# Kernel optimization log

Measured on AMD Instinct MI355X. Metric: run time of the kernel, lower is better.

The kernel has to match this reference:

```python
import jax, jax.numpy as jnp
import numpy as np

EPS = 1e-6  # EPSILON in the original (undefined there; small stabilizer)
MS = 1      # max_shift_size
FEAT = 128  # memory_feature_size


def setup_inputs() -> dict:
    key = jax.random.key(0)
    ks = jax.random.split(key, 17)
    B, V, E, H, N, F = 64, 10000, 256, 512, 8192, FEAT
    G = 4 * H
    s = 0.02  # param init scale
    return {
        'x': jax.random.randint(ks[0], (B,), 0, V),
        'h': jax.random.normal(ks[1], (B, H)) * 0.1,
        'c': jax.random.normal(ks[2], (B, H)) * 0.1,
        'w_read': jax.random.uniform(ks[3], (B, N)),
        'w_write': jax.random.uniform(ks[4], (B, N)),
        'bank': jax.random.normal(ks[5], (B, N, F)),
        'emb': jax.random.normal(ks[6], (V, E)) * s,
        'W_ih': jax.random.normal(ks[7], (G, E)) * s,
        'b_ih': jnp.zeros((G,)),
        'W_hh': jax.random.normal(ks[8], (G, H)) * s,
        'b_hh': jnp.zeros((G,)),
        'W_read': jax.random.normal(ks[9], (134, H)) * s,
        'b_read': jnp.zeros((134,)),
        'W_write': jax.random.normal(ks[10], (390, H)) * s,
        'b_write': jnp.zeros((390,)),
        'W_out': jax.random.normal(ks[11], (V, F)) * s,
        'b_out': jnp.zeros((V,)),
    }


def _lstm_cell(xe, h, c, W_ih, b_ih, W_hh, b_hh):
    g = xe @ W_ih.T + b_ih + h @ W_hh.T + b_hh  # [B, 4H]
    i, f, gg, o = jnp.split(g, 4, axis=1)
    c2 = jax.nn.sigmoid(f) * c + jax.nn.sigmoid(i) * jnp.tanh(gg)
    h2 = jax.nn.sigmoid(o) * jnp.tanh(c2)
    return h2, c2


def _head_move(bank, w_prev, k, b, g, s, r):
    # content addressing: cosine similarity of key vs each memory row
    mE = bank + EPS                       # [B, N, F]
    kE = k[:, None, :] + EPS              # [B, 1, F]
    num = jnp.sum(mE * kE, axis=-1)       # [B, N]
    den = jnp.linalg.norm(mE, axis=-1) * jnp.linalg.norm(kE, axis=-1)
    sim = num / jnp.maximum(den, 1e-8)
    w = jax.nn.softmax(b * sim, axis=1)
    # interpolation (as written in the source: w + (1-g)*w_prev)
    w = w + (1.0 - g) * w_prev
    # circular shift by location addressing (vectorized conv over modulo pad)
    N = w.shape[1]
    idx = (jnp.arange(N)[:, None] + jnp.arange(-MS, MS + 1)[None, :]) % N  # [N, K]
    w = jnp.einsum('bnk,bk->bn', w[:, idx], s)
    # sharpen
    wr = w ** r
    return wr / (jnp.sum(wr, axis=1, keepdims=True) + EPS)


def _interpret_read(h, W, b):
    o = h @ W.T + b
    F = FEAT
    k = o[:, :F]
    beta = jax.nn.softplus(o[:, F:F + 1])
    g = jax.nn.sigmoid(o[:, F + 1:F + 2])
    s = jax.nn.softmax(o[:, F + 2:F + 2 + (2 * MS + 1)], axis=1)
    r = 1.0 + jax.nn.softplus(o[:, F + 2 + (2 * MS + 1):F + 3 + (2 * MS + 1)])
    return k, beta, g, s, r


def _interpret_write(h, W, b):
    o = h @ W.T + b
    F = FEAT
    k, beta, g, s, r = _interpret_read(h, W[:F + 3 + (2 * MS + 1)], b[:F + 3 + (2 * MS + 1)])
    base = F + 3 + (2 * MS + 1)
    e = jax.nn.sigmoid(o[:, base:base + F])
    a = o[:, base + F:base + 2 * F]
    return k, beta, g, s, r, e, a


def reference(x, h, c, w_read, w_write, bank, emb, W_ih, b_ih, W_hh, b_hh,
              W_read, b_read, W_write, b_write, W_out, b_out):
    # controller
    xe = emb[x]                                  # [B, E]
    h2, c2 = _lstm_cell(xe, h, c, W_ih, b_ih, W_hh, b_hh)
    # write head + memory write
    k, beta, g, s, r, e, a = _interpret_write(h2, W_write, b_write)
    ww = _head_move(bank, w_write, k, beta, g, s, r)   # [B, N]
    bank2 = bank * (1.0 - ww[:, :, None] * e[:, None, :]) + ww[:, :, None] * a[:, None, :]
    # read head + memory read (uses updated bank)
    k, beta, g, s, r = _interpret_read(h2, W_read, b_read)
    wr = _head_move(bank2, w_read, k, beta, g, s, r)
    rvec = jnp.sum(wr[:, :, None] * bank2, axis=1)     # [B, F]
    return rvec @ W_out.T + b_out                      # [B, V]
```

## Files before the change

kernel.cpp:

```cpp
#include <hip/hip_runtime.h>
#include <math.h>

#define BB   64
#define NN   8192
#define FF   128
#define HH   512
#define GG   2048
#define EE   256
#define VV   10000
#define EPSF 1e-6f

static constexpr size_t OFF_XT    = 0;
static constexpr size_t OFF_GPART = 49152;
static constexpr size_t OFF_H2T   = 311296;
static constexpr size_t OFF_HPART = 344064;
static constexpr size_t OFF_PAR   = 411136;
static constexpr size_t OFF_ZW    = 445952;
static constexpr size_t OFF_Q4    = 970240;
static constexpr size_t OFF_Q1    = 3067392;
static constexpr size_t OFF_WR    = 3591680;
static constexpr size_t OFF_WRWW  = 4115968;
static constexpr size_t OFF_PT    = 4640256;
static constexpr size_t OFF_T3    = 5164544;
static constexpr size_t OFF_RVEC  = 5164608;

__device__ __forceinline__ float sigmoidf_(float x){ return 1.f/(1.f + __expf(-x)); }
__device__ __forceinline__ float softplusf_(float x){ return (x > 20.f) ? x : log1pf(__expf(x)); }

__global__ __launch_bounds__(256) void gather_xt_kernel(
    const int* __restrict__ x, const float* __restrict__ h,
    const float* __restrict__ emb, float* __restrict__ Xt)
{
  const int idx = blockIdx.x*256 + threadIdx.x;
  const int k = idx >> 6, b = idx & 63;
  float v = (k < EE) ? emb[(size_t)x[b]*EE + k] : h[(size_t)b*HH + (k - EE)];
  Xt[(size_t)k*64 + b] = v;
}

__global__ __launch_bounds__(256) void lstm_gates_kernel(
    const float* __restrict__ Xt, const float* __restrict__ Wih,
    const float* __restrict__ Whh, float* __restrict__ gpart)
{
  const int tid = threadIdx.x;
  const int lane = tid & 63;
  const int gw = __builtin_amdgcn_readfirstlane(blockIdx.x*4 + (tid >> 6));
  const int jg = gw >> 1, kc = gw & 1;
  const int j0 = jg << 2;
  float a0=0.f, a1=0.f, a2=0.f, a3=0.f;
  if (kc == 0){
    const float* w0 = Wih + (size_t)(j0+0)*EE;
    const float* w1 = Wih + (size_t)(j0+1)*EE;
    const float* w2 = Wih + (size_t)(j0+2)*EE;
    const float* w3 = Wih + (size_t)(j0+3)*EE;
    #pragma unroll 4
    for (int k = 0; k < EE; ++k){
      const float xv = Xt[(size_t)k*64 + lane];
      a0 = fmaf(w0[k],xv,a0); a1 = fmaf(w1[k],xv,a1);
      a2 = fmaf(w2[k],xv,a2); a3 = fmaf(w3[k],xv,a3);
    }
    const float* v0 = Whh + (size_t)(j0+0)*HH;
    const float* v1 = Whh + (size_t)(j0+1)*HH;
    const float* v2 = Whh + (size_t)(j0+2)*HH;
    const float* v3 = Whh + (size_t)(j0+3)*HH;
    #pragma unroll 4
    for (int k = 0; k < 128; ++k){
      const float xv = Xt[(size_t)(EE+k)*64 + lane];
      a0 = fmaf(v0[k],xv,a0); a1 = fmaf(v1[k],xv,a1);
      a2 = fmaf(v2[k],xv,a2); a3 = fmaf(v3[k],xv,a3);
    }
  } else {
    const float* v0 = Whh + (size_t)(j0+0)*HH;
    const float* v1 = Whh + (size_t)(j0+1)*HH;
    const float* v2 = Whh + (size_t)(j0+2)*HH;
    const float* v3 = Whh + (size_t)(j0+3)*HH;
    #pragma unroll 4
    for (int k = 128; k < 512; ++k){
      const float xv = Xt[(size_t)(EE+k)*64 + lane];
      a0 = fmaf(v0[k],xv,a0); a1 = fmaf(v1[k],xv,a1);
      a2 = fmaf(v2[k],xv,a2); a3 = fmaf(v3[k],xv,a3);
    }
  }
  float* gp = gpart + (size_t)kc*131072 + (size_t)j0*64 + lane;
  gp[0] = a0; gp[64] = a1; gp[128] = a2; gp[192] = a3;
}

__global__ __launch_bounds__(256) void lstm_act_kernel(
    const float* __restrict__ gpart, const float* __restrict__ bih,
    const float* __restrict__ bhh, const float* __restrict__ c,
    float* __restrict__ h2t)
{
  const int idx = blockIdx.x*256 + threadIdx.x;
  const int bb = idx & 63, hh = idx >> 6;
  #define GSUM(j) (gpart[(size_t)(j)*64+bb] + gpart[(size_t)131072+(size_t)(j)*64+bb] + bih[j] + bhh[j])
  const float gi = GSUM(hh);
  const float gf = GSUM(512+hh);
  const float gg = GSUM(1024+hh);
  const float go = GSUM(1536+hh);
  #undef GSUM
  const float c0 = c[(size_t)bb*HH + hh];
  const float c2 = sigmoidf_(gf)*c0 + sigmoidf_(gi)*tanhf(gg);
  h2t[(size_t)hh*64 + bb] = sigmoidf_(go)*tanhf(c2);
}

__global__ __launch_bounds__(256) void head_gemm_kernel(
    const float* __restrict__ h2t, const float* __restrict__ Ww,
    const float* __restrict__ Wr, float* __restrict__ hpart)
{
  const int tid = threadIdx.x;
  const int lane = tid & 63;
  const int gw = __builtin_amdgcn_readfirstlane(blockIdx.x*4 + (tid >> 6));
  const int jg = gw >> 1, kc = gw & 1;
  if (jg >= 131) return;
  const int j0 = jg << 2;
  const float* w0 = (j0+0 < 390) ? (Ww + (size_t)(j0+0)*HH) : (Wr + (size_t)(j0+0-390)*HH);
  const float* w1 = (j0+1 < 390) ? (Ww + (size_t)(j0+1)*HH) : (Wr + (size_t)(j0+1-390)*HH);
  const float* w2 = (j0+2 < 390) ? (Ww + (size_t)(j0+2)*HH) : (Wr + (size_t)(j0+2-390)*HH);
  const float* w3 = (j0+3 < 390) ? (Ww + (size_t)(j0+3)*HH) : (Wr + (size_t)(j0+3-390)*HH);
  const int k0 = kc << 8;
  float a0=0.f, a1=0.f, a2=0.f, a3=0.f;
  #pragma unroll 4
  for (int k = k0; k < k0+256; ++k){
    const float xv = h2t[(size_t)k*64 + lane];
    a0 = fmaf(w0[k],xv,a0); a1 = fmaf(w1[k],xv,a1);
    a2 = fmaf(w2[k],xv,a2); a3 = fmaf(w3[k],xv,a3);
  }
  float* hp = hpart + (size_t)kc*33536 + (size_t)j0*64 + lane;
  hp[0] = a0; hp[64] = a1; hp[128] = a2; hp[192] = a3;
}

__global__ void interpret_kernel(const float* __restrict__ hp,
                                 const float* __restrict__ bw,
                                 const float* __restrict__ br,
                                 float* __restrict__ params)
{
  const int b = blockIdx.x, l = threadIdx.x;
  float* P = params + (size_t)b*544;
  #define OC(j) (hp[(size_t)(j)*64+b] + hp[(size_t)33536+(size_t)(j)*64+b])
  float skw = 0.f, skr = 0.f, sakr = 0.f, sa2 = 0.f;
  #pragma unroll
  for (int f = l; f < 128; f += 64){
    float kwE = OC(f) + bw[f] + EPSF;
    float ee  = sigmoidf_(OC(134+f) + bw[134+f]);
    float aa  = OC(262+f) + bw[262+f];
    float krE = OC(390+f) + br[f] + EPSF;
    P[f] = kwE; P[128+f] = krE; P[256+f] = aa; P[384+f] = ee;
    skw = fmaf(kwE,kwE,skw); skr = fmaf(krE,krE,skr);
    sakr = fmaf(aa,krE,sakr); sa2 = fmaf(aa,aa,sa2);
  }
  #pragma unroll
  for (int m = 32; m >= 1; m >>= 1){
    skw += __shfl_xor(skw,m); skr += __shfl_xor(skr,m);
    sakr += __shfl_xor(sakr,m); sa2 += __shfl_xor(sa2,m);
  }
  if (l == 0){
    P[512+0] = softplusf_(OC(128) + bw[128]);
    P[512+1] = sigmoidf_(OC(129) + bw[129]);
    {
      float x0 = OC(130)+bw[130], x1 = OC(131)+bw[131], x2 = OC(132)+bw[132];
      float mm = fmaxf(x0, fmaxf(x1, x2));
      float e0 = __expf(x0-mm), e1 = __expf(x1-mm), e2 = __expf(x2-mm);
      float s = e0+e1+e2;
      P[512+2] = e0/s; P[512+3] = e1/s; P[512+4] = e2/s;
    }
    P[512+5] = 1.f + softplusf_(OC(133) + bw[133]);
    P[512+6] = softplusf_(OC(518) + br[128]);
    P[512+7] = sigmoidf_(OC(519) + br[129]);
    {
      float x0 = OC(520)+br[130], x1 = OC(521)+br[131], x2 = OC(522)+br[132];
      float mm = fmaxf(x0, fmaxf(x1, x2));
      float e0 = __expf(x0-mm), e1 = __expf(x1-mm), e2 = __expf(x2-mm);
      float s = e0+e1+e2;
      P[512+8] = e0/s; P[512+9] = e1/s; P[512+10] = e2/s;
    }
    P[512+11] = 1.f + softplusf_(OC(523) + br[133]);
    P[512+12] = sqrtf(skw); P[512+13] = sqrtf(skr);
    P[512+14] = sakr;       P[512+15] = sa2;
  }
  #undef OC
}

__global__ __launch_bounds__(256) void pass_a_kernel(
    const float* __restrict__ bank, const float* __restrict__ params,
    float* __restrict__ zw, float4* __restrict__ q4, float* __restrict__ q1)
{
  const int blk = blockIdx.x;
  const int b = blk >> 5, chunk = blk & 31;
  const int tid = threadIdx.x;
  const int wv = tid >> 6, lane = tid & 63;
  const int fslot = lane & 7, rsub = lane >> 3;
  const float* P = params + (size_t)b*544;
  float kw[16], kr[16], av[16], ev[16];
  #pragma unroll
  for (int i = 0; i < 4; ++i){
    #pragma unroll
    for (int j = 0; j < 4; ++j){
      const int idx = 32*i + 4*fslot + j;
      kw[4*i+j] = P[idx];     kr[4*i+j] = P[128+idx];
      av[4*i+j] = P[256+idx]; ev[4*i+j] = P[384+idx];
    }
  }
  const float beta_w = P[512+0], nkw = P[512+12];
  const float C_akr = P[512+14], Ca2 = P[512+15];
  const int eoff = 4*fslot;

  for (int it = 0; it < 8; it += 2){
    const int n0 = (chunk << 8) + (it << 5) + (wv << 3) + rsub;
    const size_t rowA = (size_t)b*NN + n0;
    const size_t rowB = rowA + 32;
    const float* pA = bank + rowA*FF + eoff;
    const float* pB = bank + rowB*FF + eoff;
    float va[16], vb[16];
    #pragma unroll
    for (int i = 0; i < 4; ++i)
      *reinterpret_cast<float4*>(&va[4*i]) = *reinterpret_cast<const float4*>(pA + 32*i);
    #pragma unroll
    for (int i = 0; i < 4; ++i)
      *reinterpret_cast<float4*>(&vb[4*i]) = *reinterpret_cast<const float4*>(pB + 32*i);

    #pragma unroll
    for (int half = 0; half < 2; ++half){
      const float* mv = (half == 0) ? va : vb;
      const size_t row = (half == 0) ? rowA : rowB;
      float s1=0.f,s2=0.f,s3=0.f,s4=0.f,s5=0.f,s6=0.f,s7=0.f,s8=0.f;
      #pragma unroll
      for (int i = 0; i < 16; ++i){
        const float m = mv[i], u = m + EPSF, em = ev[i]*m;
        s1 = fmaf(u,kw[i],s1);  s2 = fmaf(u,u,s2);
        s3 = fmaf(u,kr[i],s3);  s4 = fmaf(em,kr[i],s4);
        s5 = fmaf(u,av[i],s5);  s6 = fmaf(u,em,s6);
        s7 = fmaf(av[i],em,s7); s8 = fmaf(em,em,s8);
      }
      #pragma unroll
      for (int mm = 1; mm < 8; mm <<= 1){
        s1 += __shfl_xor(s1,mm); s2 += __shfl_xor(s2,mm);
        s3 += __shfl_xor(s3,mm); s4 += __shfl_xor(s4,mm);
        s5 += __shfl_xor(s5,mm); s6 += __shfl_xor(s6,mm);
        s7 += __shfl_xor(s7,mm); s8 += __shfl_xor(s8,mm);
      }
      if (fslot == 0){
        const float sim = s1 / fmaxf(sqrtf(s2)*nkw, 1e-8f);
        zw[row] = beta_w * sim;
        q4[row] = make_float4(s2, s3, C_akr - s4, s5 - s6);
        q1[row] = Ca2 - 2.f*s7 + s8;
      }
    }
  }
}

__device__ __forceinline__ float blockMaxF(float v, float* red, int tid){
  #pragma unroll
  for (int m = 32; m >= 1; m >>= 1) v = fmaxf(v, __shfl_xor(v,m));
  if ((tid & 63) == 0) red[tid >> 6] = v;
  __syncthreads();
  if (tid < 64){
    float x = (tid < 16) ? red[tid] : -1e30f;
    #pragma unroll
    for (int m = 8; m >= 1; m >>= 1) x = fmaxf(x, __shfl_xor(x,m));
    if (tid == 0) red[16] = x;
  }
  __syncthreads();
  return red[16];
}
__device__ __forceinline__ float blockSumF(float v, float* red, int tid){
  #pragma unroll
  for (int m = 32; m >= 1; m >>= 1) v += __shfl_xor(v,m);
  if ((tid & 63) == 0) red[tid >> 6] = v;
  __syncthreads();
  if (tid < 64){
    float x = (tid < 16) ? red[tid] : 0.f;
    #pragma unroll
    for (int m = 8; m >= 1; m >>= 1) x += __shfl_xor(x,m);
    if (tid == 0) red[16] = x;
  }
  __syncthreads();
  return red[16];
}

__global__ __launch_bounds__(1024) void head_pipeline_kernel(
    const float* __restrict__ zw, const float4* __restrict__ q4,
    const float* __restrict__ q1,
    const float* __restrict__ w_write, const float* __restrict__ w_read,
    const float* __restrict__ params,
    float* __restrict__ wrg, float* __restrict__ wrwwg, float* __restrict__ T3g)
{
  __shared__ float wa[NN];
  __shared__ float red[20];
  const int b = blockIdx.x;
  const int tid = threadIdx.x;
  const float* P = params + (size_t)b*544 + 512;
  const float g_w = P[1], sw0 = P[2], sw1 = P[3], sw2 = P[4], r_w = P[5];
  const float beta_r = P[6], g_r = P[7], sr0 = P[8], sr1 = P[9], sr2 = P[10], r_r = P[11];
  const float nkr = P[13];
  const size_t base = (size_t)b*NN;

  float  zv[8], q1v[8], wwr[8], wrd[8];
  float4 qv[8];
  #pragma unroll
  for (int i = 0; i < 8; ++i){ int n = tid + (i<<10); zv[i]  = zw[base+n]; }
  #pragma unroll
  for (int i = 0; i < 8; ++i){ int n = tid + (i<<10); qv[i]  = q4[base+n]; }
  #pragma unroll
  for (int i = 0; i < 8; ++i){ int n = tid + (i<<10); q1v[i] = q1[base+n]; }
  #pragma unroll
  for (int i = 0; i < 8; ++i){ int n = tid + (i<<10); wwr[i] = w_write[base+n]; }
  #pragma unroll
  for (int i = 0; i < 8; ++i){ int n = tid + (i<<10); wrd[i] = w_read[base+n]; }

  float cv[8], wwv[8];

  float lm = -1e30f;
  #pragma unroll
  for (int i = 0; i < 8; ++i) lm = fmaxf(lm, zv[i]);
  float M = blockMaxF(lm, red, tid);
  float ls = 0.f;
  #pragma unroll
  for (int i = 0; i < 8; ++i){ zv[i] = __expf(zv[i]-M); ls += zv[i]; }
  float S = blockSumF(ls, red, tid);
  const float invS = 1.f/S;
  #pragma unroll
  for (int i = 0; i < 8; ++i){ int n = tid + (i<<10); wa[n] = zv[i]*invS + (1.f-g_w)*wwr[i]; }
  __syncthreads();
  #pragma unroll
  for (int i = 0; i < 8; ++i){ int n = tid + (i<<10);
    cv[i] = sw0*wa[(n+NN-1)&(NN-1)] + sw1*wa[n] + sw2*wa[(n+1)&(NN-1)]; }
  __syncthreads();
  float lp = 0.f;
  #pragma unroll
  for (int i = 0; i < 8; ++i){ cv[i] = __expf(r_w*__logf(cv[i])); lp += cv[i]; }
  float Sp = blockSumF(lp, red, tid);
  float inv = 1.f/(Sp + EPSF);
  #pragma unroll
  for (int i = 0; i < 8; ++i) wwv[i] = cv[i]*inv;

  lm = -1e30f;
  #pragma unroll
  for (int i = 0; i < 8; ++i){
    const float ww = wwv[i];
    const float num = qv[i].y + ww*qv[i].z;
    const float d2  = qv[i].x + 2.f*ww*qv[i].w + ww*ww*q1v[i];
    const float den = sqrtf(d2)*nkr;
    zv[i] = beta_r * (num / fmaxf(den, 1e-8f));
    lm = fmaxf(lm, zv[i]);
  }
  M = blockMaxF(lm, red, tid);
  ls = 0.f;
  #pragma unroll
  for (int i = 0; i < 8; ++i){ zv[i] = __expf(zv[i]-M); ls += zv[i]; }
  S = blockSumF(ls, red, tid);
  const float invS2 = 1.f/S;
  #pragma unroll
  for (int i = 0; i < 8; ++i){ int n = tid + (i<<10); wa[n] = zv[i]*invS2 + (1.f-g_r)*wrd[i]; }
  __syncthreads();
  #pragma unroll
  for (int i = 0; i < 8; ++i){ int n = tid + (i<<10);
    cv[i] = sr0*wa[(n+NN-1)&(NN-1)] + sr1*wa[n] + sr2*wa[(n+1)&(NN-1)]; }
  __syncthreads();
  float lp2 = 0.f;
  #pragma unroll
  for (int i = 0; i < 8; ++i){ cv[i] = __expf(r_r*__logf(cv[i])); lp2 += cv[i]; }
  float Sp2 = blockSumF(lp2, red, tid);
  inv = 1.f/(Sp2 + EPSF);
  float t3 = 0.f;
  #pragma unroll
  for (int i = 0; i < 8; ++i){
    int n = tid + (i<<10);
    const float wr_ = cv[i]*inv;
    wrg[base+n] = wr_;
    const float xx = wr_*wwv[i];
    wrwwg[base+n] = xx;
    t3 += xx;
  }
  float T3 = blockSumF(t3, red, tid);
  if (tid == 0) T3g[b] = T3;
}

__global__ __launch_bounds__(256) void pass_d_kernel(
    const float* __restrict__ bank, const float* __restrict__ wrg,
    const float* __restrict__ wrwwg, float* __restrict__ pT)
{
  const int blk = 2047 - blockIdx.x;
  const int b = blk >> 5, chunk = blk & 31;
  const int tid = threadIdx.x;
  const int st = tid >> 5, li = tid & 31;
  float4 a1 = make_float4(0.f,0.f,0.f,0.f);
  float4 a2 = make_float4(0.f,0.f,0.f,0.f);
  for (int it = 28; it >= 0; it -= 4){
    float w1v[4], w2v[4];
    float4 mv[4];
    #pragma unroll
    for (int u = 0; u < 4; ++u){
      const int n = (chunk << 8) + ((it+u) << 3) + st;
      const size_t row = (size_t)b*NN + n;
      w1v[u] = wrg[row];
      w2v[u] = wrwwg[row];
      mv[u] = reinterpret_cast<const float4*>(bank + row*FF)[li];
    }
    #pragma unroll
    for (int u = 0; u < 4; ++u){
      a1.x = fmaf(w1v[u],mv[u].x,a1.x); a1.y = fmaf(w1v[u],mv[u].y,a1.y);
      a1.z = fmaf(w1v[u],mv[u].z,a1.z); a1.w = fmaf(w1v[u],mv[u].w,a1.w);
      a2.x = fmaf(w2v[u],mv[u].x,a2.x); a2.y = fmaf(w2v[u],mv[u].y,a2.y);
      a2.z = fmaf(w2v[u],mv[u].z,a2.z); a2.w = fmaf(w2v[u],mv[u].w,a2.w);
    }
  }
  __shared__ float lds[8*256];
  *reinterpret_cast<float4*>(&lds[st*256 + li*4]) = a1;
  *reinterpret_cast<float4*>(&lds[st*256 + 128 + li*4]) = a2;
  __syncthreads();
  float s = 0.f;
  #pragma unroll
  for (int k = 0; k < 8; ++k) s += lds[k*256 + tid];
  pT[(size_t)blk*256 + tid] = s;
}

__global__ __launch_bounds__(256) void rvec_kernel(
    const float* __restrict__ pT, const float* __restrict__ params,
    const float* __restrict__ T3g, float* __restrict__ rvec)
{
  const int gid = blockIdx.x*256 + threadIdx.x;
  const int b = gid >> 7, f = gid & 127;
  float t1 = 0.f, t2 = 0.f;
  for (int cc = 0; cc < 32; ++cc){
    const float* p = pT + (size_t)((b<<5) + cc)*256;
    t1 += p[f]; t2 += p[128+f];
  }
  const float* P = params + (size_t)b*544;
  rvec[gid] = t1 - P[384+f]*t2 + P[256+f]*T3g[b];
}

__global__ __launch_bounds__(256) void out_gemm_kernel(
    const float* __restrict__ rvec, const float* __restrict__ Wout,
    const float* __restrict__ bout, float* __restrict__ out)
{
  const int tid = threadIdx.x;
  const int wv = __builtin_amdgcn_readfirstlane(tid >> 6);
  const int lane = tid & 63;
  const int j0 = blockIdx.x*32 + wv*8;
  float acc[8];
  #pragma unroll
  for (int jj = 0; jj < 8; ++jj){ int j = j0 + jj; acc[jj] = (j < VV) ? bout[j] : 0.f; }
  for (int fc = 0; fc < 128; fc += 32){
    float rv[32];
    #pragma unroll
    for (int i = 0; i < 32; ++i) rv[i] = rvec[lane*128 + fc + i];
    #pragma unroll
    for (int jj = 0; jj < 8; ++jj){
      const int j = j0 + jj;
      if (j < VV){
        const float* w = Wout + (size_t)j*128 + fc;
        #pragma unroll
        for (int i = 0; i < 32; ++i) acc[jj] = fmaf(w[i], rv[i], acc[jj]);
      }
    }
  }
  #pragma unroll
  for (int jj = 0; jj < 8; ++jj){
    int j = j0 + jj;
    if (j < VV) out[(size_t)lane*VV + j] = acc[jj];
  }
}

extern "C" void kernel_launch(void* const* d_in, const int* in_sizes, int n_in,
                              void* d_out, int out_size, void* d_ws, size_t ws_size,
                              hipStream_t stream)
{
  const int*   x       = (const int*)  d_in[0];
  const float* h       = (const float*)d_in[1];
  const float* c       = (const float*)d_in[2];
  const float* w_read  = (const float*)d_in[3];
  const float* w_write = (const float*)d_in[4];
  const float* bank    = (const float*)d_in[5];
  const float* emb     = (const float*)d_in[6];
  const float* Wih     = (const float*)d_in[7];
  const float* bih     = (const float*)d_in[8];
  const float* Whh     = (const float*)d_in[9];
  const float* bhh     = (const float*)d_in[10];
  const float* Wr      = (const float*)d_in[11];
  const float* br      = (const float*)d_in[12];
  const float* Ww      = (const float*)d_in[13];
  const float* bw      = (const float*)d_in[14];
  const float* Wout    = (const float*)d_in[15];
  const float* bout    = (const float*)d_in[16];
  float* out = (float*)d_out;
  float* ws  = (float*)d_ws;

  float* Xt    = ws + OFF_XT;
  float* gpart = ws + OFF_GPART;
  float* h2t   = ws + OFF_H2T;
  float* hpart = ws + OFF_HPART;
  float* par   = ws + OFF_PAR;
  float* zwp   = ws + OFF_ZW;
  float4* q4p  = reinterpret_cast<float4*>(ws + OFF_Q4);
  float* q1p   = ws + OFF_Q1;
  float* wrp   = ws + OFF_WR;
  float* wrwwp = ws + OFF_WRWW;
  float* pTp   = ws + OFF_PT;
  float* T3p   = ws + OFF_T3;
  float* rvp   = ws + OFF_RVEC;

  hipLaunchKernelGGL(gather_xt_kernel,     dim3(192),  dim3(256), 0, stream, x, h, emb, Xt);
  hipLaunchKernelGGL(lstm_gates_kernel,    dim3(256),  dim3(256), 0, stream, Xt, Wih, Whh, gpart);
  hipLaunchKernelGGL(lstm_act_kernel,      dim3(128),  dim3(256), 0, stream, gpart, bih, bhh, c, h2t);
  hipLaunchKernelGGL(head_gemm_kernel,     dim3(66),   dim3(256), 0, stream, h2t, Ww, Wr, hpart);
  hipLaunchKernelGGL(interpret_kernel,     dim3(64),   dim3(64),  0, stream, hpart, bw, br, par);
  hipLaunchKernelGGL(pass_a_kernel,        dim3(2048), dim3(256), 0, stream, bank, par, zwp, q4p, q1p);
  hipLaunchKernelGGL(head_pipeline_kernel, dim3(64),   dim3(1024),0, stream, zwp, q4p, q1p, w_write, w_read, par, wrp, wrwwp, T3p);
  hipLaunchKernelGGL(pass_d_kernel,        dim3(2048), dim3(256), 0, stream, bank, wrp, wrwwp, pTp);
  hipLaunchKernelGGL(rvec_kernel,          dim3(32),   dim3(256), 0, stream, pTp, par, T3p, rvp);
  hipLaunchKernelGGL(out_gemm_kernel,      dim3(313),  dim3(256), 0, stream, rvp, Wout, bout, out);
}
```

Baseline: 196.5 us.

## Fuse controller and head-parameter kernels into one cooperative kernel with grid syncs

Merges the five small pre-processing kernels (embedding gather, LSTM gates, LSTM activation, head GEMM, interpret) into a single cooperative launch of 256 blocks, using grid-wide syncs between the stages. The aim is to remove four kernel launch boundaries and their gaps on these tiny latency-bound stages. In exchange it adds grid.sync barriers, which carry their own cost, and it depends on all 256 blocks being co-resident for the cooperative launch.

```diff
diff --git a/kernel.cpp b/kernel.cpp
--- a/kernel.cpp
+++ b/kernel.cpp
@@ -1,5 +1,8 @@
 #include <hip/hip_runtime.h>
+#include <hip/hip_cooperative_groups.h>
 #include <math.h>
+
+namespace cg = cooperative_groups;
 
 #define BB   64
 #define NN   8192
@@ -27,156 +30,157 @@
 __device__ __forceinline__ float sigmoidf_(float x){ return 1.f/(1.f + __expf(-x)); }
 __device__ __forceinline__ float softplusf_(float x){ return (x > 20.f) ? x : log1pf(__expf(x)); }
 
-__global__ __launch_bounds__(256) void gather_xt_kernel(
+__global__ __launch_bounds__(256) void fused_pre_kernel(
     const int* __restrict__ x, const float* __restrict__ h,
-    const float* __restrict__ emb, float* __restrict__ Xt)
-{
-  const int idx = blockIdx.x*256 + threadIdx.x;
-  const int k = idx >> 6, b = idx & 63;
-  float v = (k < EE) ? emb[(size_t)x[b]*EE + k] : h[(size_t)b*HH + (k - EE)];
-  Xt[(size_t)k*64 + b] = v;
-}
-
-__global__ __launch_bounds__(256) void lstm_gates_kernel(
-    const float* __restrict__ Xt, const float* __restrict__ Wih,
-    const float* __restrict__ Whh, float* __restrict__ gpart)
-{
-  const int tid = threadIdx.x;
+    const float* __restrict__ emb,
+    const float* __restrict__ Wih, const float* __restrict__ bih,
+    const float* __restrict__ Whh, const float* __restrict__ bhh,
+    const float* __restrict__ c,
+    const float* __restrict__ Ww, const float* __restrict__ bw,
+    const float* __restrict__ Wr, const float* __restrict__ br,
+    float* __restrict__ Xt, float* __restrict__ gpart,
+    float* __restrict__ h2t, float* __restrict__ hpart,
+    float* __restrict__ params)
+{
+  cg::grid_group grid = cg::this_grid();
+  const int tid  = threadIdx.x;
+  const int gtid = blockIdx.x*256 + tid;
   const int lane = tid & 63;
-  const int gw = __builtin_amdgcn_readfirstlane(blockIdx.x*4 + (tid >> 6));
-  const int jg = gw >> 1, kc = gw & 1;
-  const int j0 = jg << 2;
-  float a0=0.f, a1=0.f, a2=0.f, a3=0.f;
-  if (kc == 0){
-    const float* w0 = Wih + (size_t)(j0+0)*EE;
-    const float* w1 = Wih + (size_t)(j0+1)*EE;
-    const float* w2 = Wih + (size_t)(j0+2)*EE;
-    const float* w3 = Wih + (size_t)(j0+3)*EE;
-    #pragma unroll 4
-    for (int k = 0; k < EE; ++k){
-      const float xv = Xt[(size_t)k*64 + lane];
-      a0 = fmaf(w0[k],xv,a0); a1 = fmaf(w1[k],xv,a1);
-      a2 = fmaf(w2[k],xv,a2); a3 = fmaf(w3[k],xv,a3);
-    }
-    const float* v0 = Whh + (size_t)(j0+0)*HH;
-    const float* v1 = Whh + (size_t)(j0+1)*HH;
-    const float* v2 = Whh + (size_t)(j0+2)*HH;
-    const float* v3 = Whh + (size_t)(j0+3)*HH;
-    #pragma unroll 4
-    for (int k = 0; k < 128; ++k){
-      const float xv = Xt[(size_t)(EE+k)*64 + lane];
-      a0 = fmaf(v0[k],xv,a0); a1 = fmaf(v1[k],xv,a1);
-      a2 = fmaf(v2[k],xv,a2); a3 = fmaf(v3[k],xv,a3);
-    }
-  } else {
-    const float* v0 = Whh + (size_t)(j0+0)*HH;
-    const float* v1 = Whh + (size_t)(j0+1)*HH;
-    const float* v2 = Whh + (size_t)(j0+2)*HH;
-    const float* v3 = Whh + (size_t)(j0+3)*HH;
-    #pragma unroll 4
-    for (int k = 128; k < 512; ++k){
-      const float xv = Xt[(size_t)(EE+k)*64 + lane];
-      a0 = fmaf(v0[k],xv,a0); a1 = fmaf(v1[k],xv,a1);
-      a2 = fmaf(v2[k],xv,a2); a3 = fmaf(v3[k],xv,a3);
-    }
-  }
-  float* gp = gpart + (size_t)kc*131072 + (size_t)j0*64 + lane;
-  gp[0] = a0; gp[64] = a1; gp[128] = a2; gp[192] = a3;
-}
-
-__global__ __launch_bounds__(256) void lstm_act_kernel(
-    const float* __restrict__ gpart, const float* __restrict__ bih,
-    const float* __restrict__ bhh, const float* __restrict__ c,
-    float* __restrict__ h2t)
-{
-  const int idx = blockIdx.x*256 + threadIdx.x;
-  const int bb = idx & 63, hh = idx >> 6;
-  #define GSUM(j) (gpart[(size_t)(j)*64+bb] + gpart[(size_t)131072+(size_t)(j)*64+bb] + bih[j] + bhh[j])
-  const float gi = GSUM(hh);
-  const float gf = GSUM(512+hh);
-  const float gg = GSUM(1024+hh);
-  const float go = GSUM(1536+hh);
-  #undef GSUM
-  const float c0 = c[(size_t)bb*HH + hh];
-  const float c2 = sigmoidf_(gf)*c0 + sigmoidf_(gi)*tanhf(gg);
-  h2t[(size_t)hh*64 + bb] = sigmoidf_(go)*tanhf(c2);
-}
-
-__global__ __launch_bounds__(256) void head_gemm_kernel(
-    const float* __restrict__ h2t, const float* __restrict__ Ww,
-    const float* __restrict__ Wr, float* __restrict__ hpart)
-{
-  const int tid = threadIdx.x;
-  const int lane = tid & 63;
-  const int gw = __builtin_amdgcn_readfirstlane(blockIdx.x*4 + (tid >> 6));
-  const int jg = gw >> 1, kc = gw & 1;
-  if (jg >= 131) return;
-  const int j0 = jg << 2;
-  const float* w0 = (j0+0 < 390) ? (Ww + (size_t)(j0+0)*HH) : (Wr + (size_t)(j0+0-390)*HH);
-  const float* w1 = (j0+1 < 390) ? (Ww + (size_t)(j0+1)*HH) : (Wr + (size_t)(j0+1-390)*HH);
-  const float* w2 = (j0+2 < 390) ? (Ww + (size_t)(j0+2)*HH) : (Wr + (size_t)(j0+2-390)*HH);
-  const float* w3 = (j0+3 < 390) ? (Ww + (size_t)(j0+3)*HH) : (Wr + (size_t)(j0+3-390)*HH);
-  const int k0 = kc << 8;
-  float a0=0.f, a1=0.f, a2=0.f, a3=0.f;
-  #pragma unroll 4
-  for (int k = k0; k < k0+256; ++k){
-    const float xv = h2t[(size_t)k*64 + lane];
-    a0 = fmaf(w0[k],xv,a0); a1 = fmaf(w1[k],xv,a1);
-    a2 = fmaf(w2[k],xv,a2); a3 = fmaf(w3[k],xv,a3);
-  }
-  float* hp = hpart + (size_t)kc*33536 + (size_t)j0*64 + lane;
-  hp[0] = a0; hp[64] = a1; hp[128] = a2; hp[192] = a3;
-}
-
-__global__ void interpret_kernel(const float* __restrict__ hp,
-                                 const float* __restrict__ bw,
-                                 const float* __restrict__ br,
-                                 float* __restrict__ params)
-{
-  const int b = blockIdx.x, l = threadIdx.x;
-  float* P = params + (size_t)b*544;
-  #define OC(j) (hp[(size_t)(j)*64+b] + hp[(size_t)33536+(size_t)(j)*64+b])
-  float skw = 0.f, skr = 0.f, sakr = 0.f, sa2 = 0.f;
-  #pragma unroll
-  for (int f = l; f < 128; f += 64){
-    float kwE = OC(f) + bw[f] + EPSF;
-    float ee  = sigmoidf_(OC(134+f) + bw[134+f]);
-    float aa  = OC(262+f) + bw[262+f];
-    float krE = OC(390+f) + br[f] + EPSF;
-    P[f] = kwE; P[128+f] = krE; P[256+f] = aa; P[384+f] = ee;
-    skw = fmaf(kwE,kwE,skw); skr = fmaf(krE,krE,skr);
-    sakr = fmaf(aa,krE,sakr); sa2 = fmaf(aa,aa,sa2);
-  }
-  #pragma unroll
-  for (int m = 32; m >= 1; m >>= 1){
-    skw += __shfl_xor(skw,m); skr += __shfl_xor(skr,m);
-    sakr += __shfl_xor(sakr,m); sa2 += __shfl_xor(sa2,m);
-  }
-  if (l == 0){
-    P[512+0] = softplusf_(OC(128) + bw[128]);
-    P[512+1] = sigmoidf_(OC(129) + bw[129]);
-    {
-      float x0 = OC(130)+bw[130], x1 = OC(131)+bw[131], x2 = OC(132)+bw[132];
-      float mm = fmaxf(x0, fmaxf(x1, x2));
-      float e0 = __expf(x0-mm), e1 = __expf(x1-mm), e2 = __expf(x2-mm);
-      float s = e0+e1+e2;
-      P[512+2] = e0/s; P[512+3] = e1/s; P[512+4] = e2/s;
-    }
-    P[512+5] = 1.f + softplusf_(OC(133) + bw[133]);
-    P[512+6] = softplusf_(OC(518) + br[128]);
-    P[512+7] = sigmoidf_(OC(519) + br[129]);
-    {
-      float x0 = OC(520)+br[130], x1 = OC(521)+br[131], x2 = OC(522)+br[132];
-      float mm = fmaxf(x0, fmaxf(x1, x2));
-      float e0 = __expf(x0-mm), e1 = __expf(x1-mm), e2 = __expf(x2-mm);
-      float s = e0+e1+e2;
-      P[512+8] = e0/s; P[512+9] = e1/s; P[512+10] = e2/s;
-    }
-    P[512+11] = 1.f + softplusf_(OC(523) + br[133]);
-    P[512+12] = sqrtf(skw); P[512+13] = sqrtf(skr);
-    P[512+14] = sakr;       P[512+15] = sa2;
-  }
-  #undef OC
+
+  if (gtid < 49152){
+    const int k = gtid >> 6, b = gtid & 63;
+    float v = (k < EE) ? emb[(size_t)x[b]*EE + k] : h[(size_t)b*HH + (k - EE)];
+    Xt[(size_t)k*64 + b] = v;
+  }
+  grid.sync();
+
+  {
+    const int gw = __builtin_amdgcn_readfirstlane(blockIdx.x*4 + (tid >> 6));
+    const int jg = gw >> 1, kc = gw & 1;
+    const int j0 = jg << 2;
+    float a0=0.f, a1=0.f, a2=0.f, a3=0.f;
+    if (kc == 0){
+      const float* w0 = Wih + (size_t)(j0+0)*EE;
+      const float* w1 = Wih + (size_t)(j0+1)*EE;
+      const float* w2 = Wih + (size_t)(j0+2)*EE;
+      const float* w3 = Wih + (size_t)(j0+3)*EE;
+      #pragma unroll 4
+      for (int k = 0; k < EE; ++k){
+        const float xv = Xt[(size_t)k*64 + lane];
+        a0 = fmaf(w0[k],xv,a0); a1 = fmaf(w1[k],xv,a1);
+        a2 = fmaf(w2[k],xv,a2); a3 = fmaf(w3[k],xv,a3);
+      }
+      const float* v0 = Whh + (size_t)(j0+0)*HH;
+      const float* v1 = Whh + (size_t)(j0+1)*HH;
+      const float* v2 = Whh + (size_t)(j0+2)*HH;
+      const float* v3 = Whh + (size_t)(j0+3)*HH;
+      #pragma unroll 4
+      for (int k = 0; k < 128; ++k){
+        const float xv = Xt[(size_t)(EE+k)*64 + lane];
+        a0 = fmaf(v0[k],xv,a0); a1 = fmaf(v1[k],xv,a1);
+        a2 = fmaf(v2[k],xv,a2); a3 = fmaf(v3[k],xv,a3);
+      }
+    } else {
+      const float* v0 = Whh + (size_t)(j0+0)*HH;
+      const float* v1 = Whh + (size_t)(j0+1)*HH;
+      const float* v2 = Whh + (size_t)(j0+2)*HH;
+      const float* v3 = Whh + (size_t)(j0+3)*HH;
+      #pragma unroll 4
+      for (int k = 128; k < 512; ++k){
+        const float xv = Xt[(size_t)(EE+k)*64 + lane];
+        a0 = fmaf(v0[k],xv,a0); a1 = fmaf(v1[k],xv,a1);
+        a2 = fmaf(v2[k],xv,a2); a3 = fmaf(v3[k],xv,a3);
+      }
+    }
+    float* gp = gpart + (size_t)kc*131072 + (size_t)j0*64 + lane;
+    gp[0] = a0; gp[64] = a1; gp[128] = a2; gp[192] = a3;
+  }
+  grid.sync();
+
+  if (gtid < 32768){
+    const int bb = gtid & 63, hh = gtid >> 6;
+    #define GSUM(j) (gpart[(size_t)(j)*64+bb] + gpart[(size_t)131072+(size_t)(j)*64+bb] + bih[j] + bhh[j])
+    const float gi = GSUM(hh);
+    const float gf = GSUM(512+hh);
+    const float gg = GSUM(1024+hh);
+    const float go = GSUM(1536+hh);
+    #undef GSUM
+    const float c0 = c[(size_t)bb*HH + hh];
+    const float c2 = sigmoidf_(gf)*c0 + sigmoidf_(gi)*tanhf(gg);
+    h2t[(size_t)hh*64 + bb] = sigmoidf_(go)*tanhf(c2);
+  }
+  grid.sync();
+
+  {
+    const int gw = __builtin_amdgcn_readfirstlane(blockIdx.x*4 + (tid >> 6));
+    const int jg = gw >> 1, kc = gw & 1;
+    if (jg < 131){
+      const int j0 = jg << 2;
+      const float* w0 = (j0+0 < 390) ? (Ww + (size_t)(j0+0)*HH) : (Wr + (size_t)(j0+0-390)*HH);
+      const float* w1 = (j0+1 < 390) ? (Ww + (size_t)(j0+1)*HH) : (Wr + (size_t)(j0+1-390)*HH);
+      const float* w2 = (j0+2 < 390) ? (Ww + (size_t)(j0+2)*HH) : (Wr + (size_t)(j0+2-390)*HH);
+      const float* w3 = (j0+3 < 390) ? (Ww + (size_t)(j0+3)*HH) : (Wr + (size_t)(j0+3-390)*HH);
+      const int k0 = kc << 8;
+      float a0=0.f, a1=0.f, a2=0.f, a3=0.f;
+      #pragma unroll 4
+      for (int k = k0; k < k0+256; ++k){
+        const float xv = h2t[(size_t)k*64 + lane];
+        a0 = fmaf(w0[k],xv,a0); a1 = fmaf(w1[k],xv,a1);
+        a2 = fmaf(w2[k],xv,a2); a3 = fmaf(w3[k],xv,a3);
+      }
+      float* hp = hpart + (size_t)kc*33536 + (size_t)j0*64 + lane;
+      hp[0] = a0; hp[64] = a1; hp[128] = a2; hp[192] = a3;
+    }
+  }
+  grid.sync();
+
+  if (blockIdx.x < 64 && tid < 64){
+    const int b = blockIdx.x, l = tid;
+    const float* hp = hpart;
+    float* P = params + (size_t)b*544;
+    #define OC(j) (hp[(size_t)(j)*64+b] + hp[(size_t)33536+(size_t)(j)*64+b])
+    float skw = 0.f, skr = 0.f, sakr = 0.f, sa2 = 0.f;
+    #pragma unroll
+    for (int f = l; f < 128; f += 64){
+      float kwE = OC(f) + bw[f] + EPSF;
+      float ee  = sigmoidf_(OC(134+f) + bw[134+f]);
+      float aa  = OC(262+f) + bw[262+f];
+      float krE = OC(390+f) + br[f] + EPSF;
+      P[f] = kwE; P[128+f] = krE; P[256+f] = aa; P[384+f] = ee;
+      skw = fmaf(kwE,kwE,skw); skr = fmaf(krE,krE,skr);
+      sakr = fmaf(aa,krE,sakr); sa2 = fmaf(aa,aa,sa2);
+    }
+    #pragma unroll
+    for (int m = 32; m >= 1; m >>= 1){
+      skw += __shfl_xor(skw,m); skr += __shfl_xor(skr,m);
+      sakr += __shfl_xor(sakr,m); sa2 += __shfl_xor(sa2,m);
+    }
+    if (l == 0){
+      P[512+0] = softplusf_(OC(128) + bw[128]);
+      P[512+1] = sigmoidf_(OC(129) + bw[129]);
+      {
+        float x0 = OC(130)+bw[130], x1 = OC(131)+bw[131], x2 = OC(132)+bw[132];
+        float mm = fmaxf(x0, fmaxf(x1, x2));
+        float e0 = __expf(x0-mm), e1 = __expf(x1-mm), e2 = __expf(x2-mm);
+        float s = e0+e1+e2;
+        P[512+2] = e0/s; P[512+3] = e1/s; P[512+4] = e2/s;
+      }
+      P[512+5] = 1.f + softplusf_(OC(133) + bw[133]);
+      P[512+6] = softplusf_(OC(518) + br[128]);
+      P[512+7] = sigmoidf_(OC(519) + br[129]);
+      {
+        float x0 = OC(520)+br[130], x1 = OC(521)+br[131], x2 = OC(522)+br[132];
+        float mm = fmaxf(x0, fmaxf(x1, x2));
+        float e0 = __expf(x0-mm), e1 = __expf(x1-mm), e2 = __expf(x2-mm);
+        float s = e0+e1+e2;
+        P[512+8] = e0/s; P[512+9] = e1/s; P[512+10] = e2/s;
+      }
+      P[512+11] = 1.f + softplusf_(OC(523) + br[133]);
+      P[512+12] = sqrtf(skw); P[512+13] = sqrtf(skr);
+      P[512+14] = sakr;       P[512+15] = sa2;
+    }
+    #undef OC
+  }
 }
 
 __global__ __launch_bounds__(256) void pass_a_kernel(
@@ -498,11 +502,15 @@
   float* T3p   = ws + OFF_T3;
   float* rvp   = ws + OFF_RVEC;
 
-  hipLaunchKernelGGL(gather_xt_kernel,     dim3(192),  dim3(256), 0, stream, x, h, emb, Xt);
-  hipLaunchKernelGGL(lstm_gates_kernel,    dim3(256),  dim3(256), 0, stream, Xt, Wih, Whh, gpart);
-  hipLaunchKernelGGL(lstm_act_kernel,      dim3(128),  dim3(256), 0, stream, gpart, bih, bhh, c, h2t);
-  hipLaunchKernelGGL(head_gemm_kernel,     dim3(66),   dim3(256), 0, stream, h2t, Ww, Wr, hpart);
-  hipLaunchKernelGGL(interpret_kernel,     dim3(64),   dim3(64),  0, stream, hpart, bw, br, par);
+  void* pre_args[] = {
+    (void*)&x, (void*)&h, (void*)&emb,
+    (void*)&Wih, (void*)&bih, (void*)&Whh, (void*)&bhh,
+    (void*)&c, (void*)&Ww, (void*)&bw, (void*)&Wr, (void*)&br,
+    (void*)&Xt, (void*)&gpart, (void*)&h2t, (void*)&hpart, (void*)&par
+  };
+  hipLaunchCooperativeKernel((const void*)fused_pre_kernel,
+                             dim3(256), dim3(256), pre_args, 0, stream);
+
   hipLaunchKernelGGL(pass_a_kernel,        dim3(2048), dim3(256), 0, stream, bank, par, zwp, q4p, q1p);
   hipLaunchKernelGGL(head_pipeline_kernel, dim3(64),   dim3(1024),0, stream, zwp, q4p, q1p, w_write, w_read, par, wrp, wrwwp, T3p);
   hipLaunchKernelGGL(pass_d_kernel,        dim3(2048), dim3(256), 0, stream, bank, wrp, wrwwp, pTp);
```

Measured after the change: 295.7 us (median of 2 runs). 1.5x slower.
